# Optimization experiments

Hardware: AMD Instinct MI355X
Metric: run time of the kernel (lower is better)

Reference implementation:

```python
import jax, jax.numpy as jnp
import numpy as np

C_IN, C_OUT = 64, 32
SD, RFF = 2, 16
RF = 0.05          # receptive_field percentile
TEMP = 1.0
EPS = 1e-8
RFF_STD = 6.0


def setup_inputs() -> dict:
    key = jax.random.key(0)
    ks = jax.random.split(key, 10)
    B_, T, V, Q = 2, 4, 2048, 512
    x = jax.random.normal(ks[0], (B_, T, V, C_IN), dtype=jnp.float32)
    pos = jax.random.uniform(ks[1], (V, SD), dtype=jnp.float32)
    query_pos = jax.random.uniform(ks[2], (Q, SD), dtype=jnp.float32)
    s = 1.0 / np.sqrt(C_IN)
    W_lin = jax.random.uniform(ks[3], (C_IN, C_IN), minval=-s, maxval=s, dtype=jnp.float32)
    b_lin = jax.random.uniform(ks[4], (C_IN,), minval=-s, maxval=s, dtype=jnp.float32)
    Bmat = RFF_STD * jax.random.normal(ks[5], (SD, RFF), dtype=jnp.float32)
    s1 = 1.0 / np.sqrt(32)
    W1 = jax.random.uniform(ks[6], (32, 32), minval=-s1, maxval=s1, dtype=jnp.float32)
    b1 = jax.random.uniform(ks[7], (32,), minval=-s1, maxval=s1, dtype=jnp.float32)
    W2 = jax.random.uniform(ks[8], (C_IN * C_OUT, 32), minval=-s1, maxval=s1, dtype=jnp.float32)
    sf = np.sqrt(3.0 / C_IN)
    filt = jax.random.uniform(ks[9], (C_IN * C_OUT,), minval=-sf, maxval=sf, dtype=jnp.float32)
    bias = jnp.zeros((C_OUT,), dtype=jnp.float32)
    return {"x": x, "pos": pos, "query_pos": query_pos, "W_lin": W_lin, "b_lin": b_lin,
            "Bmat": Bmat, "W1": W1, "b1": b1, "W2": W2, "filt": filt, "bias": bias}


def reference(x, pos, query_pos, W_lin, b_lin, Bmat, W1, b1, W2, filt, bias):
    # pairwise periodic displacement / squared distance
    dist = query_pos[:, None, :] - pos[None, :, :]            # (Q, V, 2)
    dist = (dist + 0.5) % 1.0 - 0.5                           # periodic wrap
    edist = jnp.sum(dist ** 2, axis=-1)                       # (Q, V)
    # quantile threshold -> max neighbourhood size (eager, data-dependent like torch)
    thr = jnp.quantile(edist, RF, axis=-1, keepdims=True)     # linear interpolation, as torch
    K = int(jnp.max(jnp.sum(edist <= thr, axis=-1)))
    _, ind = jax.lax.top_k(-edist, K)                         # (Q, K) nearest neighbours
    # gather per-query neighbour displacements / distances
    d_g = jnp.take_along_axis(dist, ind[..., None], axis=1)   # (Q, K, 2)
    e_g = jnp.take_along_axis(edist, ind, axis=1)[..., None]  # (Q, K, 1)
    e_g = e_g - jnp.min(e_g, axis=-2, keepdims=True)
    e_g = e_g / (jnp.max(e_g, axis=-2, keepdims=True) + EPS)
    k_dist = jax.nn.softmax(-e_g / TEMP, axis=-2)             # (Q, K, 1)
    # random Fourier features + kernel MLP
    proj = 2.0 * jnp.pi * (d_g @ Bmat)                        # (Q, K, 16)
    kfeat = jnp.concatenate([jnp.sin(proj), jnp.cos(proj)], axis=-1)  # (Q, K, 32)
    h = jax.nn.gelu(kfeat @ W1.T + b1, approximate=False)
    ker = (h @ W2.T + filt) * k_dist                          # (Q, K, C_IN*C_OUT)
    ker = ker.reshape(ker.shape[0], ker.shape[1], C_IN, C_OUT)
    # point-wise linear on features, then gather + contract
    xl = x @ W_lin.T + b_lin                                  # (B, T, V, C_IN)
    xg = xl[:, :, ind, :]                                     # (B, T, Q, K, C_IN)
    return jnp.einsum('qvcd,btqvc->btqd', ker, xg) + bias     # (B, T, Q, C_OUT)
```

## Files before the change

### kernel.cpp

```cpp
#include <hip/hip_runtime.h>

#define K_SEL 103
typedef unsigned long long ull_t;
typedef _Float16 f16x8 __attribute__((ext_vector_type(8)));
typedef _Float16 f16x4 __attribute__((ext_vector_type(4)));
typedef float f32x4 __attribute__((ext_vector_type(4)));

__global__ __launch_bounds__(512, 6) void k12(const float* __restrict__ pos,
                                              const float* __restrict__ qpos,
                                              const float* __restrict__ Bmat,
                                              const float* __restrict__ W1,
                                              const float* __restrict__ b1,
                                              _Float16* __restrict__ Hh,
                                              int* __restrict__ indg,
                                              float* __restrict__ invtot,
                                              const float* __restrict__ x,
                                              const float* __restrict__ W,
                                              const float* __restrict__ b,
                                              _Float16* __restrict__ xlh,
                                              const float* __restrict__ W2,
                                              const float* __restrict__ filt,
                                              _Float16* __restrict__ W2th) {
    __shared__ __align__(16) unsigned char smem[31008];
    const int tid = threadIdx.x;
    const int bid = blockIdx.x;
    const int lane = tid & 63;
    const int wid = tid >> 6;

    if (bid >= 512) {
        const int bb = bid - 512;
        float* Wt = (float*)smem;
        if (tid < 264) {
            int t = bb * 264 + tid;
            int d = t & 31;
            int e = t >> 5;
            int c = e & 63;
            int j = e >> 6;
            float v = (j < 32) ? W2[(c * 32 + d) * 32 + j] : filt[c * 32 + d];
            W2th[d * 2112 + e] = (_Float16)v;
        }
        for (int t = tid; t < 4096; t += 512)
            Wt[(t & 63) * 65 + (t >> 6)] = W[t];
        __syncthreads();
        const int i = tid & 63;
        const int sub = tid >> 6;
        const float bi = b[i];
        #pragma unroll
        for (int rr = 0; rr < 2; ++rr) {
            const int r0 = bb * 64 + rr * 32 + sub * 4;
            float acc0 = bi, acc1 = bi, acc2 = bi, acc3 = bi;
            const float* xr = x + (size_t)r0 * 64;
            #pragma unroll 4
            for (int jj = 0; jj < 16; ++jj) {
                float4 v0 = *(const float4*)(xr + 0 * 64 + jj * 4);
                float4 v1 = *(const float4*)(xr + 1 * 64 + jj * 4);
                float4 v2 = *(const float4*)(xr + 2 * 64 + jj * 4);
                float4 v3 = *(const float4*)(xr + 3 * 64 + jj * 4);
                float w0 = Wt[(jj * 4 + 0) * 65 + i];
                float w1 = Wt[(jj * 4 + 1) * 65 + i];
                float w2 = Wt[(jj * 4 + 2) * 65 + i];
                float w3 = Wt[(jj * 4 + 3) * 65 + i];
                acc0 += v0.x * w0 + v0.y * w1 + v0.z * w2 + v0.w * w3;
                acc1 += v1.x * w0 + v1.y * w1 + v1.z * w2 + v1.w * w3;
                acc2 += v2.x * w0 + v2.y * w1 + v2.z * w2 + v2.w * w3;
                acc3 += v3.x * w0 + v3.y * w1 + v3.z * w2 + v3.w * w3;
            }
            xlh[(size_t)(r0 + 0) * 64 + i] = (_Float16)acc0;
            xlh[(size_t)(r0 + 1) * 64 + i] = (_Float16)acc1;
            xlh[(size_t)(r0 + 2) * 64 + i] = (_Float16)acc2;
            xlh[(size_t)(r0 + 3) * 64 + i] = (_Float16)acc3;
        }
        return;
    }

    const int q = bid;
    unsigned* ebits   = (unsigned*)(smem);
    unsigned* hist    = (unsigned*)(smem + 8192);
    _Float16* Hs      = (_Float16*)(smem + 8192);
    float*    W1t     = (float*)(smem + 24576);
    float*    b1s     = (float*)(smem + 28800);
    float*    Bm      = (float*)(smem + 28928);
    int*      sel_v   = (int*)(smem + 29056);
    float*    sel_e   = (float*)(smem + 29472);
    ull_t*    bnd     = (ull_t*)(smem + 29888);
    int*      counters= (int*)(smem + 30912);
    int*      info    = (int*)(smem + 30920);
    float*    wred    = (float*)(smem + 30928);
    float*    emax_s  = (float*)(smem + 30960);
    unsigned* wscan   = (unsigned*)(smem + 30964);

    for (int t = tid; t < 1024; t += 512)
        W1t[(t & 31) * 33 + (t >> 5)] = W1[t];
    if (tid < 32) { b1s[tid] = b1[tid]; Bm[tid] = Bmat[tid]; }
    if (tid < 2)  counters[tid] = 0;
    for (int t = tid; t < 1024; t += 512) ((uint4*)hist)[t] = make_uint4(0, 0, 0, 0);
    const float qp0 = qpos[q * 2 + 0];
    const float qp1 = qpos[q * 2 + 1];
    __syncthreads();

    float lmin = 1e30f;
    for (int v = tid; v < 2048; v += 512) {
        float2 p = ((const float2*)pos)[v];
        float d0 = qp0 - p.x;
        float d1 = qp1 - p.y;
        d0 += 0.5f; d0 -= floorf(d0); d0 -= 0.5f;
        d1 += 0.5f; d1 -= floorf(d1); d1 -= 0.5f;
        float e = d0 * d0 + d1 * d1;
        ebits[v] = __float_as_uint(e);
        lmin = fminf(lmin, e);
        int bb2 = (int)(e * 8192.0f); bb2 = (bb2 > 4095) ? 4095 : bb2;
        atomicAdd(&hist[bb2], 1u);
    }
    #pragma unroll
    for (int off = 32; off > 0; off >>= 1)
        lmin = fminf(lmin, __shfl_xor(lmin, off, 64));
    if (lane == 0) wred[wid] = lmin;
    __syncthreads();
    float e_min = wred[0];
    #pragma unroll
    for (int w2 = 1; w2 < 8; ++w2) e_min = fminf(e_min, wred[w2]);

    unsigned lsum = 0;
    #pragma unroll
    for (int i = 0; i < 8; ++i) lsum += hist[tid * 8 + i];
    unsigned vq = lsum;
    #pragma unroll
    for (int off = 1; off < 64; off <<= 1) {
        unsigned n = __shfl_up(vq, off, 64);
        if (lane >= off) vq += n;
    }
    if (lane == 63) wscan[wid] = vq;
    __syncthreads();
    unsigned base = 0;
    for (int w2 = 0; w2 < wid; ++w2) base += wscan[w2];
    unsigned cum = base + vq - lsum;
    #pragma unroll
    for (int i = 0; i < 8; ++i) {
        unsigned cnt = hist[tid * 8 + i];
        if (cum <= 102u && 102u < cum + cnt) { info[0] = tid * 8 + i; info[1] = (int)cum; }
        cum += cnt;
    }
    __syncthreads();
    const int Bstar = info[0];
    const int L = info[1];
    const int need = K_SEL - L;

    {
        f16x8 z = {0, 0, 0, 0, 0, 0, 0, 0};
        for (int t = tid; t < 768; t += 512) ((f16x8*)Hs)[t] = z;
    }
    for (int v = tid; v < 2048; v += 512) {
        unsigned bb2 = ebits[v];
        float e = __uint_as_float(bb2);
        int bin = (int)(e * 8192.0f); bin = (bin > 4095) ? 4095 : bin;
        if (bin < Bstar) {
            int s2 = atomicAdd(&counters[0], 1);
            sel_v[s2] = v; sel_e[s2] = e;
        } else if (bin == Bstar) {
            int s2 = atomicAdd(&counters[1], 1);
            if (s2 < 128) bnd[s2] = (((ull_t)bb2) << 32) | (unsigned)v;
        }
    }
    __syncthreads();
    {
        int nb = counters[1]; if (nb > 128) nb = 128;
        if (tid < nb) {
            ull_t my = bnd[tid];
            int rank = 0;
            for (int i = 0; i < nb; ++i) rank += (bnd[i] < my);
            if (rank < need) {
                sel_v[L + rank] = (int)(unsigned)(my & 0xffffffffull);
                sel_e[L + rank] = __uint_as_float((unsigned)(my >> 32));
            }
            if (rank == need - 1)
                emax_s[0] = __uint_as_float((unsigned)(my >> 32));
        }
    }
    __syncthreads();

    const float denom = (emax_s[0] - e_min) + 1e-8f;
    float w = 0.0f;
    if (tid < K_SEL) {
        w = __expf(-(sel_e[tid] - e_min) / denom);
        sel_e[tid] = w;
    }
    float sw = w;
    #pragma unroll
    for (int off = 32; off > 0; off >>= 1)
        sw += __shfl_xor(sw, off, 64);
    if (lane == 0) wred[wid] = sw;
    __syncthreads();
    if (tid == 0) {
        float tot = 0.0f;
        #pragma unroll
        for (int w2 = 0; w2 < 8; ++w2) tot += wred[w2];
        invtot[q] = 1.0f / tot;
    }

    if (tid < 4 * K_SEL) {
        const int k = tid >> 2;
        const int io = (tid & 3) * 8;
        const int sw5 = ((tid & 3) & 1) << 5;
        const int v = sel_v[k];
        const float wk = sel_e[k];
        float2 p = ((const float2*)pos)[v];
        float d0 = qp0 - p.x;
        float d1 = qp1 - p.y;
        d0 += 0.5f; d0 -= floorf(d0); d0 -= 0.5f;
        d1 += 0.5f; d1 -= floorf(d1); d1 -= 0.5f;
        float kf[32];
        #pragma unroll
        for (int f = 0; f < 16; ++f) {
            float t = d0 * Bm[f] + d1 * Bm[16 + f];
            float r = t - rintf(t);
            kf[f]      = __builtin_amdgcn_sinf(r);
            kf[16 + f] = __builtin_amdgcn_cosf(r);
        }
        #pragma unroll
        for (int i = io; i < io + 8; ++i) {
            float pre = b1s[i];
            #pragma unroll
            for (int jf = 0; jf < 32; ++jf) pre += kf[jf] * W1t[jf * 33 + i];
            float g = 0.5f * pre * (1.0f + erff(pre * 0.70710678118654752f));
            Hs[i * 128 + (k ^ sw5)] = (_Float16)(g * wk);
        }
        if (io == 0) {
            Hs[32 * 128 + k] = (_Float16)wk;
            indg[q * K_SEL + k] = v;
        }
    }
    __syncthreads();
    {
        _Float16* hq = Hh + (size_t)q * 6144;
        for (int t = tid; t < 768; t += 512)
            ((f16x8*)hq)[t] = ((const f16x8*)Hs)[t];
    }
}

__global__ __launch_bounds__(512, 4) void k3_main(const _Float16* __restrict__ xlh,
                                                  const _Float16* __restrict__ Hh,
                                                  const int* __restrict__ indg,
                                                  const _Float16* __restrict__ W2th,
                                                  const float* __restrict__ bias,
                                                  const float* __restrict__ invtot,
                                                  float* __restrict__ out) {
    const int q = blockIdx.x;
    const int tid = threadIdx.x;
    const int lane = tid & 63;
    const int wid = tid >> 6;
    const int h   = wid >> 2;
    const int cq  = wid & 3;
    const int n0 = lane & 15;
    const int quad = lane >> 4;

    __shared__ __align__(16) unsigned char smem[69504];
    _Float16* Xg  = (_Float16*)smem;
    _Float16* Zh8 = (_Float16*)(smem + 35072);
    int* ind_s    = (int*)(smem + 68992);
    float* red    = (float*)smem;

    const _Float16* hq = Hh + (size_t)q * 6144;
    f16x8 afr[4][3];
    #pragma unroll
    for (int ks = 0; ks < 4; ++ks)
        #pragma unroll
        for (int r = 0; r < 3; ++r)
            afr[ks][r] = *(const f16x8*)(hq + (r * 16 + n0) * 128 +
                                         ((ks * 32 + quad * 8) ^ ((n0 >> 3) << 5)));
    const float it = invtot[q];
    const int e0f = wid * 32 + quad * 8;
    f16x8 pf0 = *(const f16x8*)(W2th + (size_t)(0 * 16 + n0) * 2112 + e0f);
    f16x8 pf1 = *(const f16x8*)(W2th + (size_t)(1 * 16 + n0) * 2112 + e0f);
    if (tid < 128) {
        int kk = (tid < K_SEL) ? tid : tid - K_SEL;
        ind_s[tid] = indg[q * K_SEL + kk];
    }
    __syncthreads();

    const int m_oct = tid & 7;
    const int m_kb  = (tid >> 3) & 31;
    const int m_h   = tid >> 8;
    const int m_k0  = m_kb * 4;
    const int m_base = m_h * 8768 + m_oct * 1096 + m_k0;

    {
        f16x8 v0[4];
        #pragma unroll
        for (int i = 0; i < 4; ++i)
            v0[i] = *(const f16x8*)(xlh + ((size_t)m_h * 2048 + ind_s[m_k0 + i]) * 64 + m_oct * 8);
        #pragma unroll
        for (int jj = 0; jj < 8; ++jj) {
            f16x4 pk = {v0[0][jj], v0[1][jj], v0[2][jj], v0[3][jj]};
            *(f16x4*)(&Xg[m_base + 136 * jj]) = pk;
        }
    }
    __syncthreads();

    const int cA = cq * 16 + n0;
    const int cswz = h * 8768 + cA * 136 + ((cA >> 3) << 3);

    #pragma unroll
    for (int p = 0; p < 4; ++p) {
        f16x8 vn[4];
        if (p < 3) {
            #pragma unroll
            for (int i = 0; i < 4; ++i)
                vn[i] = *(const f16x8*)(xlh + ((size_t)(2 * (p + 1) + m_h) * 2048 + ind_s[m_k0 + i]) * 64 + m_oct * 8);
        }
        f32x4 Dz[3];
        #pragma unroll
        for (int r = 0; r < 3; ++r) Dz[r] = (f32x4){0.f, 0.f, 0.f, 0.f};
        #pragma unroll
        for (int ks = 0; ks < 4; ++ks) {
            f16x8 bfr = *(const f16x8*)(&Xg[cswz + ks * 32 + quad * 8]);
            #pragma unroll
            for (int r = 0; r < 3; ++r)
                Dz[r] = __builtin_amdgcn_mfma_f32_16x16x32_f16(afr[ks][r], bfr, Dz[r], 0, 0, 0);
        }
        __syncthreads();
        const int bt = 2 * p + h;
        #pragma unroll
        for (int r = 0; r < 3; ++r)
            #pragma unroll
            for (int reg = 0; reg < 4; ++reg) {
                int j = r * 16 + quad * 4 + reg;
                if (j < 33) Zh8[bt * 2120 + j * 64 + (cA ^ (quad << 4))] = (_Float16)Dz[r][reg];
            }
        if (p < 3) {
            #pragma unroll
            for (int jj = 0; jj < 8; ++jj) {
                f16x4 pk = {vn[0][jj], vn[1][jj], vn[2][jj], vn[3][jj]};
                *(f16x4*)(&Xg[m_base + 136 * jj]) = pk;
            }
            __syncthreads();
        }
    }
    __syncthreads();

    f32x4 D2[2][2];
    #pragma unroll
    for (int pp = 0; pp < 2; ++pp)
        #pragma unroll
        for (int dt = 0; dt < 2; ++dt) D2[pp][dt] = (f32x4){0.f, 0.f, 0.f, 0.f};
    {
        const int s = wid;
        const int ja = s >> 1;
        const int phys = (((s & 1) << 5) + quad * 8) ^ (((s >> 3) & 3) << 4);
        f16x8 a2 = {0, 0, 0, 0, 0, 0, 0, 0};
        if (n0 < 8) a2 = *(const f16x8*)(&Zh8[n0 * 2120 + ja * 64 + phys]);
        D2[0][0] = __builtin_amdgcn_mfma_f32_16x16x32_f16(a2, pf0, D2[0][0], 0, 0, 0);
        D2[0][1] = __builtin_amdgcn_mfma_f32_16x16x32_f16(a2, pf1, D2[0][1], 0, 0, 0);
    }
    int pp = 1;
    #pragma unroll 2
    for (int s = wid + 8; s < 66; s += 8) {
        const int e0 = s * 32 + quad * 8;
        const int ja = s >> 1;
        const int phys = (((s & 1) << 5) + quad * 8) ^ (((s >> 3) & 3) << 4);
        f16x8 a2 = {0, 0, 0, 0, 0, 0, 0, 0};
        if (n0 < 8) a2 = *(const f16x8*)(&Zh8[n0 * 2120 + ja * 64 + phys]);
        #pragma unroll
        for (int dt = 0; dt < 2; ++dt) {
            f16x8 bfr = *(const f16x8*)(W2th + (size_t)(dt * 16 + n0) * 2112 + e0);
            D2[pp][dt] = __builtin_amdgcn_mfma_f32_16x16x32_f16(a2, bfr, D2[pp][dt], 0, 0, 0);
        }
        pp ^= 1;
    }
    #pragma unroll
    for (int dt = 0; dt < 2; ++dt)
        D2[0][dt] = D2[0][dt] + D2[1][dt];

    if (quad < 2) {
        #pragma unroll
        for (int dt = 0; dt < 2; ++dt)
            #pragma unroll
            for (int reg = 0; reg < 4; ++reg)
                red[((wid * 2 + dt) * 8 + quad * 4 + reg) * 16 + n0] = D2[0][dt][reg];
    }
    __syncthreads();
    if (tid < 256) {
        const int bt = tid >> 5;
        const int d = tid & 31;
        const int dt = d >> 4;
        const int dn = d & 15;
        float s = 0.0f;
        #pragma unroll
        for (int w2 = 0; w2 < 8; ++w2)
            s += red[((w2 * 2 + dt) * 8 + bt) * 16 + dn];
        out[((size_t)bt * 512 + q) * 32 + d] = bias[d] + it * s;
    }
}

extern "C" void kernel_launch(void* const* d_in, const int* in_sizes, int n_in,
                              void* d_out, int out_size, void* d_ws, size_t ws_size,
                              hipStream_t stream) {
    const float* x     = (const float*)d_in[0];
    const float* pos   = (const float*)d_in[1];
    const float* qpos  = (const float*)d_in[2];
    const float* W_lin = (const float*)d_in[3];
    const float* b_lin = (const float*)d_in[4];
    const float* Bmat  = (const float*)d_in[5];
    const float* W1    = (const float*)d_in[6];
    const float* b1    = (const float*)d_in[7];
    const float* W2    = (const float*)d_in[8];
    const float* filt  = (const float*)d_in[9];
    const float* bias  = (const float*)d_in[10];
    float* out = (float*)d_out;

    float* ws = (float*)d_ws;
    _Float16* xlh    = (_Float16*)ws;
    _Float16* Hh     = (_Float16*)(ws + 524288);
    int*      indg   = (int*)(ws + 2097152);
    _Float16* W2th   = (_Float16*)(ws + 2150144);
    float*    invtot = ws + 2183936;

    k12<<<768, 512, 0, stream>>>(pos, qpos, Bmat, W1, b1, Hh, indg, invtot,
                                 x, W_lin, b_lin, xlh, W2, filt, W2th);
    k3_main<<<512, 512, 0, stream>>>(xlh, Hh, indg, W2th, bias, invtot, out);
}
```

Before: 110.1 us.

## Cache displacements in LDS, pad neighbour indices, prefetch W2 fragments

In k12, positions are loaded into registers up front and the wrapped displacements are stored in shared memory, so the feature stage no longer re-reads pos and recomputes them. Histogram bins are read as vector loads into registers. The neighbour index array is padded to 128 per query, which lets k3_main load its four indices straight from global memory into registers and drop the shared-memory staging and a barrier. The W2 fragment loop is software-pipelined one step ahead. This costs about 16KB more shared memory in k12, which may reduce occupancy, and a slightly larger workspace.

After: 109.7 us. No clear change (-0.4%).

```diff
diff --git a/kernel.cpp b/kernel.cpp
--- a/kernel.cpp
+++ b/kernel.cpp
@@ -21,7 +21,7 @@
                                               const float* __restrict__ W2,
                                               const float* __restrict__ filt,
                                               _Float16* __restrict__ W2th) {
-    __shared__ __align__(16) unsigned char smem[31008];
+    __shared__ __align__(16) unsigned char smem[47392];
     const int tid = threadIdx.x;
     const int bid = blockIdx.x;
     const int lane = tid & 63;
@@ -77,36 +77,43 @@
     unsigned* ebits   = (unsigned*)(smem);
     unsigned* hist    = (unsigned*)(smem + 8192);
     _Float16* Hs      = (_Float16*)(smem + 8192);
-    float*    W1t     = (float*)(smem + 24576);
-    float*    b1s     = (float*)(smem + 28800);
-    float*    Bm      = (float*)(smem + 28928);
-    int*      sel_v   = (int*)(smem + 29056);
-    float*    sel_e   = (float*)(smem + 29472);
-    ull_t*    bnd     = (ull_t*)(smem + 29888);
-    int*      counters= (int*)(smem + 30912);
-    int*      info    = (int*)(smem + 30920);
-    float*    wred    = (float*)(smem + 30928);
-    float*    emax_s  = (float*)(smem + 30960);
-    unsigned* wscan   = (unsigned*)(smem + 30964);
+    float2*   dpair   = (float2*)(smem + 24576);
+    float*    W1t     = (float*)(smem + 40960);
+    float*    b1s     = (float*)(smem + 45184);
+    float*    Bm      = (float*)(smem + 45312);
+    int*      sel_v   = (int*)(smem + 45440);
+    float*    sel_e   = (float*)(smem + 45856);
+    ull_t*    bnd     = (ull_t*)(smem + 46272);
+    int*      counters= (int*)(smem + 47296);
+    int*      info    = (int*)(smem + 47304);
+    float*    wred    = (float*)(smem + 47312);
+    float*    emax_s  = (float*)(smem + 47344);
+    unsigned* wscan   = (unsigned*)(smem + 47348);
+
+    float2 p4[4];
+    #pragma unroll
+    for (int i = 0; i < 4; ++i) p4[i] = ((const float2*)pos)[tid + i * 512];
+    const float qp0 = qpos[q * 2 + 0];
+    const float qp1 = qpos[q * 2 + 1];
 
     for (int t = tid; t < 1024; t += 512)
         W1t[(t & 31) * 33 + (t >> 5)] = W1[t];
     if (tid < 32) { b1s[tid] = b1[tid]; Bm[tid] = Bmat[tid]; }
     if (tid < 2)  counters[tid] = 0;
     for (int t = tid; t < 1024; t += 512) ((uint4*)hist)[t] = make_uint4(0, 0, 0, 0);
-    const float qp0 = qpos[q * 2 + 0];
-    const float qp1 = qpos[q * 2 + 1];
     __syncthreads();
 
     float lmin = 1e30f;
-    for (int v = tid; v < 2048; v += 512) {
-        float2 p = ((const float2*)pos)[v];
-        float d0 = qp0 - p.x;
-        float d1 = qp1 - p.y;
+    #pragma unroll
+    for (int i = 0; i < 4; ++i) {
+        const int v = tid + i * 512;
+        float d0 = qp0 - p4[i].x;
+        float d1 = qp1 - p4[i].y;
         d0 += 0.5f; d0 -= floorf(d0); d0 -= 0.5f;
         d1 += 0.5f; d1 -= floorf(d1); d1 -= 0.5f;
         float e = d0 * d0 + d1 * d1;
         ebits[v] = __float_as_uint(e);
+        dpair[v] = make_float2(d0, d1);
         lmin = fminf(lmin, e);
         int bb2 = (int)(e * 8192.0f); bb2 = (bb2 > 4095) ? 4095 : bb2;
         atomicAdd(&hist[bb2], 1u);
@@ -120,9 +127,16 @@
     #pragma unroll
     for (int w2 = 1; w2 < 8; ++w2) e_min = fminf(e_min, wred[w2]);
 
+    unsigned hb[8];
+    {
+        uint4 h0 = ((const uint4*)hist)[tid * 2];
+        uint4 h1 = ((const uint4*)hist)[tid * 2 + 1];
+        hb[0] = h0.x; hb[1] = h0.y; hb[2] = h0.z; hb[3] = h0.w;
+        hb[4] = h1.x; hb[5] = h1.y; hb[6] = h1.z; hb[7] = h1.w;
+    }
     unsigned lsum = 0;
     #pragma unroll
-    for (int i = 0; i < 8; ++i) lsum += hist[tid * 8 + i];
+    for (int i = 0; i < 8; ++i) lsum += hb[i];
     unsigned vq = lsum;
     #pragma unroll
     for (int off = 1; off < 64; off <<= 1) {
@@ -136,7 +150,7 @@
     unsigned cum = base + vq - lsum;
     #pragma unroll
     for (int i = 0; i < 8; ++i) {
-        unsigned cnt = hist[tid * 8 + i];
+        unsigned cnt = hb[i];
         if (cum <= 102u && 102u < cum + cnt) { info[0] = tid * 8 + i; info[1] = (int)cum; }
         cum += cnt;
     }
@@ -149,7 +163,9 @@
         f16x8 z = {0, 0, 0, 0, 0, 0, 0, 0};
         for (int t = tid; t < 768; t += 512) ((f16x8*)Hs)[t] = z;
     }
-    for (int v = tid; v < 2048; v += 512) {
+    #pragma unroll
+    for (int i = 0; i < 4; ++i) {
+        const int v = tid + i * 512;
         unsigned bb2 = ebits[v];
         float e = __uint_as_float(bb2);
         int bin = (int)(e * 8192.0f); bin = (bin > 4095) ? 4095 : bin;
@@ -203,11 +219,9 @@
         const int sw5 = ((tid & 3) & 1) << 5;
         const int v = sel_v[k];
         const float wk = sel_e[k];
-        float2 p = ((const float2*)pos)[v];
-        float d0 = qp0 - p.x;
-        float d1 = qp1 - p.y;
-        d0 += 0.5f; d0 -= floorf(d0); d0 -= 0.5f;
-        d1 += 0.5f; d1 -= floorf(d1); d1 -= 0.5f;
+        float2 dp = dpair[v];
+        const float d0 = dp.x;
+        const float d1 = dp.y;
         float kf[32];
         #pragma unroll
         for (int f = 0; f < 16; ++f) {
@@ -226,7 +240,8 @@
         }
         if (io == 0) {
             Hs[32 * 128 + k] = (_Float16)wk;
-            indg[q * K_SEL + k] = v;
+            indg[q * 128 + k] = v;
+            if (k < 128 - K_SEL) indg[q * 128 + K_SEL + k] = v;
         }
     }
     __syncthreads();
@@ -253,11 +268,19 @@
     const int n0 = lane & 15;
     const int quad = lane >> 4;
 
-    __shared__ __align__(16) unsigned char smem[69504];
+    __shared__ __align__(16) unsigned char smem[68992];
     _Float16* Xg  = (_Float16*)smem;
     _Float16* Zh8 = (_Float16*)(smem + 35072);
-    int* ind_s    = (int*)(smem + 68992);
     float* red    = (float*)smem;
+
+    const int m_oct = tid & 7;
+    const int m_kb  = (tid >> 3) & 31;
+    const int m_h   = tid >> 8;
+    const int m_k0  = m_kb * 4;
+    const int m_base = m_h * 8768 + m_oct * 1096 + m_k0;
+
+    const int4 ind4 = *(const int4*)(indg + q * 128 + m_k0);
+    int indr[4] = {ind4.x, ind4.y, ind4.z, ind4.w};
 
     const _Float16* hq = Hh + (size_t)q * 6144;
     f16x8 afr[4][3];
@@ -271,23 +294,12 @@
     const int e0f = wid * 32 + quad * 8;
     f16x8 pf0 = *(const f16x8*)(W2th + (size_t)(0 * 16 + n0) * 2112 + e0f);
     f16x8 pf1 = *(const f16x8*)(W2th + (size_t)(1 * 16 + n0) * 2112 + e0f);
-    if (tid < 128) {
-        int kk = (tid < K_SEL) ? tid : tid - K_SEL;
-        ind_s[tid] = indg[q * K_SEL + kk];
-    }
-    __syncthreads();
-
-    const int m_oct = tid & 7;
-    const int m_kb  = (tid >> 3) & 31;
-    const int m_h   = tid >> 8;
-    const int m_k0  = m_kb * 4;
-    const int m_base = m_h * 8768 + m_oct * 1096 + m_k0;
 
     {
         f16x8 v0[4];
         #pragma unroll
         for (int i = 0; i < 4; ++i)
-            v0[i] = *(const f16x8*)(xlh + ((size_t)m_h * 2048 + ind_s[m_k0 + i]) * 64 + m_oct * 8);
+            v0[i] = *(const f16x8*)(xlh + ((size_t)m_h * 2048 + indr[i]) * 64 + m_oct * 8);
         #pragma unroll
         for (int jj = 0; jj < 8; ++jj) {
             f16x4 pk = {v0[0][jj], v0[1][jj], v0[2][jj], v0[3][jj]};
@@ -305,7 +317,7 @@
         if (p < 3) {
             #pragma unroll
             for (int i = 0; i < 4; ++i)
-                vn[i] = *(const f16x8*)(xlh + ((size_t)(2 * (p + 1) + m_h) * 2048 + ind_s[m_k0 + i]) * 64 + m_oct * 8);
+                vn[i] = *(const f16x8*)(xlh + ((size_t)(2 * (p + 1) + m_h) * 2048 + indr[i]) * 64 + m_oct * 8);
         }
         f32x4 Dz[3];
         #pragma unroll
@@ -351,19 +363,29 @@
         D2[0][0] = __builtin_amdgcn_mfma_f32_16x16x32_f16(a2, pf0, D2[0][0], 0, 0, 0);
         D2[0][1] = __builtin_amdgcn_mfma_f32_16x16x32_f16(a2, pf1, D2[0][1], 0, 0, 0);
     }
+    f16x8 c0, c1;
+    {
+        const int s1 = wid + 8;
+        const int e1 = s1 * 32 + quad * 8;
+        c0 = *(const f16x8*)(W2th + (size_t)(0 * 16 + n0) * 2112 + e1);
+        c1 = *(const f16x8*)(W2th + (size_t)(1 * 16 + n0) * 2112 + e1);
+    }
     int pp = 1;
-    #pragma unroll 2
     for (int s = wid + 8; s < 66; s += 8) {
-        const int e0 = s * 32 + quad * 8;
+        const int sn = s + 8;
+        f16x8 nx0, nx1;
+        if (sn < 66) {
+            const int en = sn * 32 + quad * 8;
+            nx0 = *(const f16x8*)(W2th + (size_t)(0 * 16 + n0) * 2112 + en);
+            nx1 = *(const f16x8*)(W2th + (size_t)(1 * 16 + n0) * 2112 + en);
+        }
         const int ja = s >> 1;
         const int phys = (((s & 1) << 5) + quad * 8) ^ (((s >> 3) & 3) << 4);
         f16x8 a2 = {0, 0, 0, 0, 0, 0, 0, 0};
         if (n0 < 8) a2 = *(const f16x8*)(&Zh8[n0 * 2120 + ja * 64 + phys]);
-        #pragma unroll
-        for (int dt = 0; dt < 2; ++dt) {
-            f16x8 bfr = *(const f16x8*)(W2th + (size_t)(dt * 16 + n0) * 2112 + e0);
-            D2[pp][dt] = __builtin_amdgcn_mfma_f32_16x16x32_f16(a2, bfr, D2[pp][dt], 0, 0, 0);
-        }
+        D2[pp][0] = __builtin_amdgcn_mfma_f32_16x16x32_f16(a2, c0, D2[pp][0], 0, 0, 0);
+        D2[pp][1] = __builtin_amdgcn_mfma_f32_16x16x32_f16(a2, c1, D2[pp][1], 0, 0, 0);
+        c0 = nx0; c1 = nx1;
         pp ^= 1;
     }
     #pragma unroll
@@ -411,8 +433,8 @@
     _Float16* xlh    = (_Float16*)ws;
     _Float16* Hh     = (_Float16*)(ws + 524288);
     int*      indg   = (int*)(ws + 2097152);
-    _Float16* W2th   = (_Float16*)(ws + 2150144);
-    float*    invtot = ws + 2183936;
+    _Float16* W2th   = (_Float16*)(ws + 2162688);
+    float*    invtot = ws + 2196480;
 
     k12<<<768, 512, 0, stream>>>(pos, qpos, Bmat, W1, b1, Hh, indg, invtot,
                                  x, W_lin, b_lin, xlh, W2, filt, W2th);
```
